# Kernel tuning notes

Hardware: AMD Instinct MI355X
Metric: run time of the kernel (lower is better)

The kernel has to match this reference:

```python
import jax, jax.numpy as jnp
import numpy as np

B, S, D, R, N, H = 2, 2048, 1024, 64, 16, 16
DH = D // H  # 64


def setup_inputs() -> dict:
    key = jax.random.key(0)
    ks = jax.random.split(key, 16)
    inp = {
        "x": jax.random.normal(ks[0], (B, S, D), dtype=jnp.float32),
        "feature_q_w": jax.random.uniform(ks[1], (B, S, N), dtype=jnp.float32),
        "feature_k_w": jax.random.uniform(ks[2], (B, S, N), dtype=jnp.float32),
        "feature_v_w": jax.random.uniform(ks[3], (B, S, N), dtype=jnp.float32),
        "restore_q_w": jax.random.uniform(ks[4], (B, S, N), dtype=jnp.float32),
        "restore_k_w": jax.random.uniform(ks[5], (B, S, N), dtype=jnp.float32),
        "restore_v_w": jax.random.uniform(ks[6], (B, S, N), dtype=jnp.float32),
        # expert parameter pools (per-expert low-rank projections)
        "f_q": jax.random.normal(ks[7], (N, D, R), dtype=jnp.float32) / np.sqrt(D),
        "f_k": jax.random.normal(ks[8], (N, D, R), dtype=jnp.float32) / np.sqrt(D),
        "f_v": jax.random.normal(ks[9], (N, D, R), dtype=jnp.float32) / np.sqrt(D),
        "r_q": jax.random.normal(ks[10], (N, R, D), dtype=jnp.float32) / np.sqrt(R),
        "r_k": jax.random.normal(ks[11], (N, R, D), dtype=jnp.float32) / np.sqrt(R),
        "r_v": jax.random.normal(ks[12], (N, R, D), dtype=jnp.float32) / np.sqrt(R),
        # expand_O: nn.Linear(D, D, bias=False) weight, shape [D_out, D_in]
        "W_O": jax.random.normal(ks[13], (D, D), dtype=jnp.float32) / np.sqrt(D),
    }
    return inp


def _compress(w, F_pool, x):
    # math-equivalent to einsum('bsn,ndr->bsdr') then ('bsd,bsdr->bsr')
    # reordered to avoid the [B,S,D,R] intermediate: [B,S,N,R] instead.
    t = jnp.einsum('bsd,ndr->bsnr', x, F_pool)
    return jnp.einsum('bsn,bsnr->bsr', w, t)


def _restore(w, R_pool, h):
    # math-equivalent to einsum('bsn,nrd->bsrd') then ('bsr,bsrd->bsd')
    mix = jnp.einsum('bsr,bsn->bsnr', h, w)  # small [B,S,N,R]
    return jnp.einsum('bsnr,nrd->bsd', mix, R_pool)


def reference(x, feature_q_w, feature_k_w, feature_v_w,
              restore_q_w, restore_k_w, restore_v_w,
              f_q, f_k, f_v, r_q, r_k, r_v, W_O):
    b, s, d = x.shape
    h_q = _compress(feature_q_w, f_q, x)
    h_k = _compress(feature_k_w, f_k, x)
    h_v = _compress(feature_v_w, f_v, x)
    Q = _restore(restore_q_w, r_q, h_q)
    K = _restore(restore_k_w, r_k, h_k)
    V = _restore(restore_v_w, r_v, h_v)
    # split heads: [B,H,S,DH]
    Q = Q.reshape(b, s, H, DH).transpose(0, 2, 1, 3)
    K = K.reshape(b, s, H, DH).transpose(0, 2, 1, 3)
    V = V.reshape(b, s, H, DH).transpose(0, 2, 1, 3)
    scale = 1.0 / np.sqrt(DH)
    scores = jnp.einsum('bhqd,bhkd->bhqk', Q, K) * scale
    causal = jnp.tril(jnp.ones((s, s), dtype=bool))
    scores = jnp.where(causal, scores, jnp.float32(-1e9))
    attn = jax.nn.softmax(scores, axis=-1)
    out = jnp.einsum('bhqk,bhkd->bhqd', attn, V)
    out = out.transpose(0, 2, 1, 3).reshape(b, s, d)
    # nn.Linear(bias=False): y = x @ W_O.T
    return out @ W_O.T
```

## Files before the change

### kernel.cpp

```cpp
#include <hip/hip_runtime.h>

#define BS   4096
#define DD   1024
#define SEQ  2048
#define SLAB (BS * DD)
#define POOL (16 * 64 * 1024)

typedef unsigned short u16;
typedef __attribute__((ext_vector_type(8))) short  s16x8;
typedef __attribute__((ext_vector_type(4))) float  f32x4;

__device__ __forceinline__ u16 f2bf(float x) {
    unsigned u = __float_as_uint(x);
    return (u16)((u + 0x7fffu + ((u >> 16) & 1u)) >> 16);
}
__device__ __forceinline__ float bf2f(u16 h) { return __uint_as_float(((unsigned)h) << 16); }
__device__ __forceinline__ void bsplit(float x, u16& h, u16& l) {
    h = f2bf(x);
    l = f2bf(x - bf2f(h));
}

__global__ __launch_bounds__(256) void convert_ew(
    const float* __restrict__ in, u16* __restrict__ oh, u16* __restrict__ ol, int n4)
{
    for (int i = blockIdx.x * 256 + threadIdx.x; i < n4; i += gridDim.x * 256) {
        float4 v = ((const float4*)in)[i];
        u16 h0,h1,h2,h3, l0,l1,l2,l3;
        bsplit(v.x,h0,l0); bsplit(v.y,h1,l1); bsplit(v.z,h2,l2); bsplit(v.w,h3,l3);
        u16* ph = oh + i * 4; ph[0]=h0; ph[1]=h1; ph[2]=h2; ph[3]=h3;
        u16* pl = ol + i * 4; pl[0]=l0; pl[1]=l1; pl[2]=l2; pl[3]=l3;
    }
}

__global__ __launch_bounds__(256) void convert_tr3(
    const float* __restrict__ in0, const float* __restrict__ in1, const float* __restrict__ in2,
    u16* __restrict__ oh, u16* __restrict__ ol, int Rows, int Cols, int zPerPool)
{
    __shared__ float ts[64][65];
    const int z = blockIdx.z, pool = z / zPerPool, zi = z % zPerPool;
    const float* in = (pool == 0 ? in0 : (pool == 1 ? in1 : in2)) + (size_t)zi * Rows * Cols;
    const size_t obase = (size_t)z * Rows * Cols;
    const int r0 = blockIdx.x * 64, c0 = blockIdx.y * 64;
    const int t = threadIdx.x;

    const int rr = t >> 4, c4 = (t & 15) * 4;
    #pragma unroll
    for (int i = 0; i < 4; ++i) {
        int r = i * 16 + rr;
        float4 v = *(const float4*)&in[(size_t)(r0 + r) * Cols + c0 + c4];
        ts[r][c4+0] = v.x; ts[r][c4+1] = v.y; ts[r][c4+2] = v.z; ts[r][c4+3] = v.w;
    }
    __syncthreads();
    const int cc = t >> 4, rq = (t & 15) * 4;
    #pragma unroll
    for (int i = 0; i < 4; ++i) {
        int c = i * 16 + cc;
        size_t o = obase + (size_t)(c0 + c) * Rows + r0 + rq;
        #pragma unroll
        for (int j = 0; j < 4; ++j) {
            u16 h, l; bsplit(ts[rq + j][c], h, l);
            oh[o + j] = h; ol[o + j] = l;
        }
    }
}

template<int OMODE>
__global__ __launch_bounds__(256, 3) void gemm_split(
    const u16* __restrict__ Ah, const u16* __restrict__ Al,
    const u16* __restrict__ Bh, const u16* __restrict__ Bl,
    float* __restrict__ Cf, u16* __restrict__ Ch, u16* __restrict__ Cl,
    long aZ, long bZ, long cZ, int K, int lda, int ldb, int ldc)
{
    __shared__ u16 sBh[128][32], sBl[128][32];

    const int t = threadIdx.x, wave = t >> 6, lane = t & 63;
    const int m0 = blockIdx.x * 128, n0 = blockIdx.y * 128;
    const long z = blockIdx.z;
    Ah += z * aZ; Al += z * aZ; Bh += z * bZ; Bl += z * bZ;

    const int lr = lane >> 2, lk = (lane & 3) * 8;
    const u16* gBh = Bh + (size_t)(n0 + wave * 16 + lr) * ldb + lk;
    const u16* gBl = Bl + (size_t)(n0 + wave * 16 + lr) * ldb + lk;

    const int fr = lane & 15, fk = (lane >> 4) * 8;
    const u16* gAh = Ah + (size_t)(m0 + (wave >> 1) * 64 + fr) * lda + fk;
    const u16* gAl = Al + (size_t)(m0 + (wave >> 1) * 64 + fr) * lda + fk;

    f32x4 acc[4][4];
    #pragma unroll
    for (int i = 0; i < 4; ++i)
        #pragma unroll
        for (int j = 0; j < 4; ++j) acc[i][j] = (f32x4){0.f, 0.f, 0.f, 0.f};

    const int br = (wave & 1) * 64 + fr;

    for (int k0 = 0; k0 < K; k0 += 32) {
        #define STG(g, s, ld) do { \
            __builtin_amdgcn_global_load_lds( \
                (const __attribute__((address_space(1))) void*)(g + k0), \
                (__attribute__((address_space(3))) void*)&s[wave * 16][0], 16, 0, 0); \
            __builtin_amdgcn_global_load_lds( \
                (const __attribute__((address_space(1))) void*)(g + k0 + (size_t)64 * ld), \
                (__attribute__((address_space(3))) void*)&s[wave * 16 + 64][0], 16, 0, 0); \
        } while (0)
        STG(gBh, sBh, ldb); STG(gBl, sBl, ldb);
        #undef STG

        s16x8 ahf[4], alf[4];
        #pragma unroll
        for (int i = 0; i < 4; ++i) {
            ahf[i] = *(const s16x8*)&gAh[(size_t)(16 * i) * lda + k0];
            alf[i] = *(const s16x8*)&gAl[(size_t)(16 * i) * lda + k0];
        }
        __syncthreads();

        #pragma unroll
        for (int j = 0; j < 4; ++j) {
            s16x8 bh = *(const s16x8*)&sBh[br + 16 * j][fk];
            s16x8 bl = *(const s16x8*)&sBl[br + 16 * j][fk];
            #pragma unroll
            for (int i = 0; i < 4; ++i)
                acc[i][j] = __builtin_amdgcn_mfma_f32_16x16x32_bf16(ahf[i], bh, acc[i][j], 0, 0, 0);
            #pragma unroll
            for (int i = 0; i < 4; ++i)
                acc[i][j] = __builtin_amdgcn_mfma_f32_16x16x32_bf16(ahf[i], bl, acc[i][j], 0, 0, 0);
            #pragma unroll
            for (int i = 0; i < 4; ++i)
                acc[i][j] = __builtin_amdgcn_mfma_f32_16x16x32_bf16(alf[i], bh, acc[i][j], 0, 0, 0);
        }
        __syncthreads();
    }

    const int row0 = m0 + (wave >> 1) * 64 + (lane >> 4) * 4;
    const int col0 = n0 + (wave & 1) * 64 + fr;
    if constexpr (OMODE == 0) {
        Cf += z * cZ;
        #pragma unroll
        for (int i = 0; i < 4; ++i)
            #pragma unroll
            for (int j = 0; j < 4; ++j)
                #pragma unroll
                for (int r = 0; r < 4; ++r)
                    Cf[(size_t)(row0 + 16 * i + r) * ldc + col0 + 16 * j] = acc[i][j][r];
    } else {
        Ch += z * cZ; Cl += z * cZ;
        #pragma unroll
        for (int i = 0; i < 4; ++i)
            #pragma unroll
            for (int j = 0; j < 4; ++j)
                #pragma unroll
                for (int r = 0; r < 4; ++r) {
                    u16 h, l; bsplit(acc[i][j][r], h, l);
                    size_t o = (size_t)(row0 + 16 * i + r) * ldc + col0 + 16 * j;
                    Ch[o] = h; Cl[o] = l;
                }
    }
}

__global__ __launch_bounds__(256) void mix3(
    u16* __restrict__ Th, u16* __restrict__ Tl,
    const float* fw0, const float* fw1, const float* fw2,
    const float* rw0, const float* rw1, const float* rw2)
{
    const int p = blockIdx.y;
    const float* fw = p == 0 ? fw0 : (p == 1 ? fw1 : fw2);
    const float* rw = p == 0 ? rw0 : (p == 1 ? rw1 : rw2);
    u16* th = Th + (size_t)p * SLAB;
    u16* tl = Tl + (size_t)p * SLAB;

    const int t = threadIdx.x;
    const int bs = blockIdx.x * 4 + (t >> 6);
    const int r = t & 63;
    const float* fwp = fw + bs * 16;
    const float* rwp = rw + bs * 16;
    u16* rowh = th + (size_t)bs * DD + r;
    u16* rowl = tl + (size_t)bs * DD + r;

    float h = 0.f;
    #pragma unroll
    for (int n = 0; n < 16; ++n) h += fwp[n] * (bf2f(rowh[n * 64]) + bf2f(rowl[n * 64]));
    #pragma unroll
    for (int n = 0; n < 16; ++n) {
        u16 hh, ll; bsplit(rwp[n] * h, hh, ll);
        rowh[n * 64] = hh; rowl[n * 64] = ll;
    }
}

__global__ __launch_bounds__(256) void attn_mfma(
    const u16* __restrict__ Qh, const u16* __restrict__ Ql,
    const u16* __restrict__ Kh, const u16* __restrict__ Kl,
    const u16* __restrict__ Vh, const u16* __restrict__ Vl,
    u16* __restrict__ Oh, u16* __restrict__ Ol)
{
    __shared__ u16 sKh[64][64], sKl[64][64];
    __shared__ u16 sVh[64][64], sVl[64][64];
    __shared__ u16 sPh[128][64], sPl[128][64];

    const int t = threadIdx.x, w = t >> 6, lane = t & 63;
    const int g = blockIdx.x;
    const int u = g & 255, v = g >> 8;
    const int bh = (v << 4) + (u >> 4);
    const int bx = v ? (15 - (u & 15)) : (u & 15);
    const int b = bh >> 4, h = bh & 15;
    const int q0 = bx * 128;
    const int l15 = lane & 15, l4 = lane >> 4;

    s16x8 qfh[2][2], qfl[2][2];
    #pragma unroll
    for (int fi = 0; fi < 2; ++fi) {
        int qr = q0 + w * 32 + fi * 16 + l15;
        size_t base = ((size_t)(b * SEQ + qr)) * DD + h * 64;
        #pragma unroll
        for (int dk = 0; dk < 2; ++dk) {
            qfh[fi][dk] = *(const s16x8*)&Qh[base + dk * 32 + l4 * 8];
            qfl[fi][dk] = *(const s16x8*)&Ql[base + dk * 32 + l4 * 8];
        }
    }

    f32x4 oacc[2][4];
    #pragma unroll
    for (int fi = 0; fi < 2; ++fi)
        #pragma unroll
        for (int dj = 0; dj < 4; ++dj) oacc[fi][dj] = (f32x4){0.f,0.f,0.f,0.f};
    float mrow[2][4], lrow[2][4];
    #pragma unroll
    for (int fi = 0; fi < 2; ++fi)
        #pragma unroll
        for (int r = 0; r < 4; ++r) { mrow[fi][r] = -1e30f; lrow[fi][r] = 0.f; }

    const int ntiles = 2 * bx + 2;
    for (int kt = 0; kt < ntiles; ++kt) {
        __syncthreads();
        #pragma unroll
        for (int it = 0; it < 2; ++it) {
            int id = it * 256 + t;
            int kr = id >> 3, dg = (id & 7) * 8;
            size_t gaddr = ((size_t)(b * SEQ + kt * 64 + kr)) * DD + h * 64 + dg;
            s16x8 kh8 = *(const s16x8*)&Kh[gaddr];
            s16x8 kl8 = *(const s16x8*)&Kl[gaddr];
            int kbyte = (dg * 2) ^ ((kr & 7) << 4);
            *(s16x8*)((char*)&sKh[kr][0] + kbyte) = kh8;
            *(s16x8*)((char*)&sKl[kr][0] + kbyte) = kl8;
            s16x8 vh8 = *(const s16x8*)&Vh[gaddr];
            s16x8 vl8 = *(const s16x8*)&Vl[gaddr];
            #pragma unroll
            for (int j = 0; j < 8; ++j) {
                int d = dg + j;
                int vbyte = (kr * 2) ^ ((d & 7) << 4);
                *(u16*)((char*)&sVh[d][0] + vbyte) = (u16)vh8[j];
                *(u16*)((char*)&sVl[d][0] + vbyte) = (u16)vl8[j];
            }
        }
        __syncthreads();

        f32x4 s[2][4];
        #pragma unroll
        for (int fi = 0; fi < 2; ++fi)
            #pragma unroll
            for (int fj = 0; fj < 4; ++fj) s[fi][fj] = (f32x4){0.f,0.f,0.f,0.f};
        #pragma unroll
        for (int fj = 0; fj < 4; ++fj) {
            int krow = fj * 16 + l15;
            #pragma unroll
            for (int dk = 0; dk < 2; ++dk) {
                int byte = ((dk * 32 + l4 * 8) * 2) ^ ((krow & 7) << 4);
                s16x8 kbh = *(const s16x8*)((const char*)&sKh[krow][0] + byte);
                s16x8 kbl = *(const s16x8*)((const char*)&sKl[krow][0] + byte);
                #pragma unroll
                for (int fi = 0; fi < 2; ++fi) {
                    s[fi][fj] = __builtin_amdgcn_mfma_f32_16x16x32_bf16(qfh[fi][dk], kbh, s[fi][fj], 0,0,0);
                    s[fi][fj] = __builtin_amdgcn_mfma_f32_16x16x32_bf16(qfh[fi][dk], kbl, s[fi][fj], 0,0,0);
                    s[fi][fj] = __builtin_amdgcn_mfma_f32_16x16x32_bf16(qfl[fi][dk], kbh, s[fi][fj], 0,0,0);
                }
            }
        }

        #pragma unroll
        for (int fi = 0; fi < 2; ++fi) {
            int qrow = q0 + w * 32 + fi * 16 + l4 * 4;
            #pragma unroll
            for (int fj = 0; fj < 4; ++fj) {
                int kcol = kt * 64 + fj * 16 + l15;
                #pragma unroll
                for (int r = 0; r < 4; ++r)
                    s[fi][fj][r] = (kcol > qrow + r) ? -1e9f : s[fi][fj][r] * 0.125f;
            }
        }

        #pragma unroll
        for (int fi = 0; fi < 2; ++fi) {
            f32x4 pm = s[fi][0];
            #pragma unroll
            for (int fj = 1; fj < 4; ++fj)
                #pragma unroll
                for (int r = 0; r < 4; ++r) pm[r] = fmaxf(pm[r], s[fi][fj][r]);
            #pragma unroll
            for (int st = 1; st < 16; st <<= 1)
                #pragma unroll
                for (int r = 0; r < 4; ++r) pm[r] = fmaxf(pm[r], __shfl_xor(pm[r], st));

            float al[4];
            #pragma unroll
            for (int r = 0; r < 4; ++r) {
                float mn = fmaxf(mrow[fi][r], pm[r]);
                al[r] = __expf(mrow[fi][r] - mn);
                mrow[fi][r] = mn;
            }
            f32x4 rs = (f32x4){0.f,0.f,0.f,0.f};
            #pragma unroll
            for (int fj = 0; fj < 4; ++fj) {
                #pragma unroll
                for (int r = 0; r < 4; ++r) {
                    float p = __expf(s[fi][fj][r] - mrow[fi][r]);
                    rs[r] += p;
                    u16 ph, pl; bsplit(p, ph, pl);
                    int prow = w * 32 + fi * 16 + l4 * 4 + r;
                    int byte = ((fj * 16 + l15) * 2) ^ ((prow & 7) << 4);
                    *(u16*)((char*)&sPh[prow][0] + byte) = ph;
                    *(u16*)((char*)&sPl[prow][0] + byte) = pl;
                }
            }
            #pragma unroll
            for (int st = 1; st < 16; st <<= 1)
                #pragma unroll
                for (int r = 0; r < 4; ++r) rs[r] += __shfl_xor(rs[r], st);
            #pragma unroll
            for (int r = 0; r < 4; ++r) {
                lrow[fi][r] = lrow[fi][r] * al[r] + rs[r];
                #pragma unroll
                for (int dj = 0; dj < 4; ++dj) oacc[fi][dj][r] *= al[r];
            }
        }

        #pragma unroll
        for (int kk = 0; kk < 2; ++kk) {
            s16x8 pah[2], pal[2];
            #pragma unroll
            for (int fi = 0; fi < 2; ++fi) {
                int prow = w * 32 + fi * 16 + l15;
                int byte = ((kk * 32 + l4 * 8) * 2) ^ ((prow & 7) << 4);
                pah[fi] = *(const s16x8*)((const char*)&sPh[prow][0] + byte);
                pal[fi] = *(const s16x8*)((const char*)&sPl[prow][0] + byte);
            }
            #pragma unroll
            for (int dj = 0; dj < 4; ++dj) {
                int vrow = dj * 16 + l15;
                int byte = ((kk * 32 + l4 * 8) * 2) ^ ((vrow & 7) << 4);
                s16x8 vbh = *(const s16x8*)((const char*)&sVh[vrow][0] + byte);
                s16x8 vbl = *(const s16x8*)((const char*)&sVl[vrow][0] + byte);
                #pragma unroll
                for (int fi = 0; fi < 2; ++fi) {
                    oacc[fi][dj] = __builtin_amdgcn_mfma_f32_16x16x32_bf16(pah[fi], vbh, oacc[fi][dj], 0,0,0);
                    oacc[fi][dj] = __builtin_amdgcn_mfma_f32_16x16x32_bf16(pah[fi], vbl, oacc[fi][dj], 0,0,0);
                    oacc[fi][dj] = __builtin_amdgcn_mfma_f32_16x16x32_bf16(pal[fi], vbh, oacc[fi][dj], 0,0,0);
                }
            }
        }
    }

    #pragma unroll
    for (int fi = 0; fi < 2; ++fi)
        #pragma unroll
        for (int r = 0; r < 4; ++r) {
            int qr = q0 + w * 32 + fi * 16 + l4 * 4 + r;
            size_t base = ((size_t)(b * SEQ + qr)) * DD + h * 64;
            float inv = 1.0f / lrow[fi][r];
            #pragma unroll
            for (int dj = 0; dj < 4; ++dj) {
                u16 hh, ll; bsplit(oacc[fi][dj][r] * inv, hh, ll);
                Oh[base + dj * 16 + l15] = hh;
                Ol[base + dj * 16 + l15] = ll;
            }
        }
}

extern "C" void kernel_launch(void* const* d_in, const int* in_sizes, int n_in,
                              void* d_out, int out_size, void* d_ws, size_t ws_size,
                              hipStream_t stream)
{
    const float* x     = (const float*)d_in[0];
    const float* fw[3] = { (const float*)d_in[1], (const float*)d_in[2], (const float*)d_in[3] };
    const float* rw[3] = { (const float*)d_in[4], (const float*)d_in[5], (const float*)d_in[6] };
    const float* fp[3] = { (const float*)d_in[7], (const float*)d_in[8], (const float*)d_in[9] };
    const float* rp[3] = { (const float*)d_in[10], (const float*)d_in[11], (const float*)d_in[12] };
    const float* Wo    = (const float*)d_in[13];
    float* out = (float*)d_out;

    u16* U    = (u16*)d_ws;
    u16* xh   = U;                  u16* xl   = xh  + SLAB;
    u16* fTh  = xl   + SLAB;        u16* fTl  = fTh + 3 * POOL;
    u16* rTh  = fTl  + 3 * POOL;    u16* rTl  = rTh + 3 * POOL;
    u16* Wh   = rTl  + 3 * POOL;    u16* Wl   = Wh  + POOL;
    u16* Th   = Wl   + POOL;        u16* Tl   = Th  + 3 * SLAB;
    u16* QKVh = Tl   + 3 * SLAB;    u16* QKVl = QKVh + 3 * SLAB;
    u16* Ohb  = xh;                 u16* Olb  = xl;

    dim3 blk(256);

    convert_ew<<<dim3(4096), blk, 0, stream>>>(x,  xh, xl, SLAB / 4);
    convert_ew<<<dim3(1024), blk, 0, stream>>>(Wo, Wh, Wl, (DD * DD) / 4);
    convert_tr3<<<dim3(16, 1, 48), blk, 0, stream>>>(fp[0], fp[1], fp[2], fTh, fTl, 1024, 64, 16);
    convert_tr3<<<dim3(16, 16, 3), blk, 0, stream>>>(rp[0], rp[1], rp[2], rTh, rTl, 1024, 1024, 1);

    gemm_split<1><<<dim3(32, 8, 3), blk, 0, stream>>>(
        xh, xl, fTh, fTl, nullptr, Th, Tl, 0, POOL, SLAB, DD, DD, DD, DD);

    mix3<<<dim3(BS / 4, 3), blk, 0, stream>>>(
        Th, Tl, fw[0], fw[1], fw[2], rw[0], rw[1], rw[2]);

    gemm_split<1><<<dim3(32, 8, 3), blk, 0, stream>>>(
        Th, Tl, rTh, rTl, nullptr, QKVh, QKVl, SLAB, POOL, SLAB, DD, DD, DD, DD);

    attn_mfma<<<dim3(512), blk, 0, stream>>>(
        QKVh, QKVl, QKVh + SLAB, QKVl + SLAB, QKVh + 2 * SLAB, QKVl + 2 * SLAB,
        Ohb, Olb);

    gemm_split<0><<<dim3(32, 8, 1), blk, 0, stream>>>(
        Ohb, Olb, Wh, Wl, out, nullptr, nullptr, 0, 0, 0, DD, DD, DD, DD);
}
```

Measured before the change: 637.4 us.

## Write V transposed from projection GEMM and read K/V directly from global in attention

```diff
diff --git a/kernel.cpp b/kernel.cpp
--- a/kernel.cpp
+++ b/kernel.cpp
@@ -69,7 +69,7 @@
     const u16* __restrict__ Ah, const u16* __restrict__ Al,
     const u16* __restrict__ Bh, const u16* __restrict__ Bl,
     float* __restrict__ Cf, u16* __restrict__ Ch, u16* __restrict__ Cl,
-    long aZ, long bZ, long cZ, int K, int lda, int ldb, int ldc)
+    long aZ, long bZ, long cZ, int K, int lda, int ldb, int ldc, int vtrans)
 {
     __shared__ u16 sBh[128][32], sBl[128][32];
 
@@ -144,16 +144,37 @@
                     Cf[(size_t)(row0 + 16 * i + r) * ldc + col0 + 16 * j] = acc[i][j][r];
     } else {
         Ch += z * cZ; Cl += z * cZ;
-        #pragma unroll
-        for (int i = 0; i < 4; ++i)
-            #pragma unroll
-            for (int j = 0; j < 4; ++j)
-                #pragma unroll
-                for (int r = 0; r < 4; ++r) {
-                    u16 h, l; bsplit(acc[i][j][r], h, l);
-                    size_t o = (size_t)(row0 + 16 * i + r) * ldc + col0 + 16 * j;
-                    Ch[o] = h; Cl[o] = l;
+        if (vtrans && z == 2) {
+            const int b_ = m0 >> 11;
+            const int h_ = (n0 + (wave & 1) * 64) >> 6;
+            #pragma unroll
+            for (int i = 0; i < 4; ++i) {
+                int srow = (m0 & (SEQ - 1)) + (wave >> 1) * 64 + (lane >> 4) * 4 + 16 * i;
+                #pragma unroll
+                for (int j = 0; j < 4; ++j) {
+                    int d = fr + 16 * j;
+                    size_t o = ((size_t)((b_ * 16 + h_) * 64 + d)) * SEQ + srow;
+                    ushort4 hv, lv;
+                    bsplit(acc[i][j][0], hv.x, lv.x);
+                    bsplit(acc[i][j][1], hv.y, lv.y);
+                    bsplit(acc[i][j][2], hv.z, lv.z);
+                    bsplit(acc[i][j][3], hv.w, lv.w);
+                    *(ushort4*)&Ch[o] = hv;
+                    *(ushort4*)&Cl[o] = lv;
                 }
+            }
+        } else {
+            #pragma unroll
+            for (int i = 0; i < 4; ++i)
+                #pragma unroll
+                for (int j = 0; j < 4; ++j)
+                    #pragma unroll
+                    for (int r = 0; r < 4; ++r) {
+                        u16 h, l; bsplit(acc[i][j][r], h, l);
+                        size_t o = (size_t)(row0 + 16 * i + r) * ldc + col0 + 16 * j;
+                        Ch[o] = h; Cl[o] = l;
+                    }
+        }
     }
 }
 
@@ -189,11 +210,9 @@
 __global__ __launch_bounds__(256) void attn_mfma(
     const u16* __restrict__ Qh, const u16* __restrict__ Ql,
     const u16* __restrict__ Kh, const u16* __restrict__ Kl,
-    const u16* __restrict__ Vh, const u16* __restrict__ Vl,
+    const u16* __restrict__ Vth, const u16* __restrict__ Vtl,
     u16* __restrict__ Oh, u16* __restrict__ Ol)
 {
-    __shared__ u16 sKh[64][64], sKl[64][64];
-    __shared__ u16 sVh[64][64], sVl[64][64];
     __shared__ u16 sPh[128][64], sPl[128][64];
 
     const int t = threadIdx.x, w = t >> 6, lane = t & 63;
@@ -230,29 +249,6 @@
 
     const int ntiles = 2 * bx + 2;
     for (int kt = 0; kt < ntiles; ++kt) {
-        __syncthreads();
-        #pragma unroll
-        for (int it = 0; it < 2; ++it) {
-            int id = it * 256 + t;
-            int kr = id >> 3, dg = (id & 7) * 8;
-            size_t gaddr = ((size_t)(b * SEQ + kt * 64 + kr)) * DD + h * 64 + dg;
-            s16x8 kh8 = *(const s16x8*)&Kh[gaddr];
-            s16x8 kl8 = *(const s16x8*)&Kl[gaddr];
-            int kbyte = (dg * 2) ^ ((kr & 7) << 4);
-            *(s16x8*)((char*)&sKh[kr][0] + kbyte) = kh8;
-            *(s16x8*)((char*)&sKl[kr][0] + kbyte) = kl8;
-            s16x8 vh8 = *(const s16x8*)&Vh[gaddr];
-            s16x8 vl8 = *(const s16x8*)&Vl[gaddr];
-            #pragma unroll
-            for (int j = 0; j < 8; ++j) {
-                int d = dg + j;
-                int vbyte = (kr * 2) ^ ((d & 7) << 4);
-                *(u16*)((char*)&sVh[d][0] + vbyte) = (u16)vh8[j];
-                *(u16*)((char*)&sVl[d][0] + vbyte) = (u16)vl8[j];
-            }
-        }
-        __syncthreads();
-
         f32x4 s[2][4];
         #pragma unroll
         for (int fi = 0; fi < 2; ++fi)
@@ -260,12 +256,11 @@
             for (int fj = 0; fj < 4; ++fj) s[fi][fj] = (f32x4){0.f,0.f,0.f,0.f};
         #pragma unroll
         for (int fj = 0; fj < 4; ++fj) {
-            int krow = fj * 16 + l15;
+            size_t kbase = ((size_t)(b * SEQ + kt * 64 + fj * 16 + l15)) * DD + h * 64;
             #pragma unroll
             for (int dk = 0; dk < 2; ++dk) {
-                int byte = ((dk * 32 + l4 * 8) * 2) ^ ((krow & 7) << 4);
-                s16x8 kbh = *(const s16x8*)((const char*)&sKh[krow][0] + byte);
-                s16x8 kbl = *(const s16x8*)((const char*)&sKl[krow][0] + byte);
+                s16x8 kbh = *(const s16x8*)&Kh[kbase + dk * 32 + l4 * 8];
+                s16x8 kbl = *(const s16x8*)&Kl[kbase + dk * 32 + l4 * 8];
                 #pragma unroll
                 for (int fi = 0; fi < 2; ++fi) {
                     s[fi][fj] = __builtin_amdgcn_mfma_f32_16x16x32_bf16(qfh[fi][dk], kbh, s[fi][fj], 0,0,0);
@@ -344,10 +339,9 @@
             }
             #pragma unroll
             for (int dj = 0; dj < 4; ++dj) {
-                int vrow = dj * 16 + l15;
-                int byte = ((kk * 32 + l4 * 8) * 2) ^ ((vrow & 7) << 4);
-                s16x8 vbh = *(const s16x8*)((const char*)&sVh[vrow][0] + byte);
-                s16x8 vbl = *(const s16x8*)((const char*)&sVl[vrow][0] + byte);
+                size_t vbase = ((size_t)(bh * 64 + dj * 16 + l15)) * SEQ + kt * 64 + kk * 32 + l4 * 8;
+                s16x8 vbh = *(const s16x8*)&Vth[vbase];
+                s16x8 vbl = *(const s16x8*)&Vtl[vbase];
                 #pragma unroll
                 for (int fi = 0; fi < 2; ++fi) {
                     oacc[fi][dj] = __builtin_amdgcn_mfma_f32_16x16x32_bf16(pah[fi], vbh, oacc[fi][dj], 0,0,0);
@@ -403,18 +397,18 @@
     convert_tr3<<<dim3(16, 16, 3), blk, 0, stream>>>(rp[0], rp[1], rp[2], rTh, rTl, 1024, 1024, 1);
 
     gemm_split<1><<<dim3(32, 8, 3), blk, 0, stream>>>(
-        xh, xl, fTh, fTl, nullptr, Th, Tl, 0, POOL, SLAB, DD, DD, DD, DD);
+        xh, xl, fTh, fTl, nullptr, Th, Tl, 0, POOL, SLAB, DD, DD, DD, DD, 0);
 
     mix3<<<dim3(BS / 4, 3), blk, 0, stream>>>(
         Th, Tl, fw[0], fw[1], fw[2], rw[0], rw[1], rw[2]);
 
     gemm_split<1><<<dim3(32, 8, 3), blk, 0, stream>>>(
-        Th, Tl, rTh, rTl, nullptr, QKVh, QKVl, SLAB, POOL, SLAB, DD, DD, DD, DD);
+        Th, Tl, rTh, rTl, nullptr, QKVh, QKVl, SLAB, POOL, SLAB, DD, DD, DD, DD, 1);
 
     attn_mfma<<<dim3(512), blk, 0, stream>>>(
         QKVh, QKVl, QKVh + SLAB, QKVl + SLAB, QKVh + 2 * SLAB, QKVl + 2 * SLAB,
         Ohb, Olb);
 
     gemm_split<0><<<dim3(32, 8, 1), blk, 0, stream>>>(
-        Ohb, Olb, Wh, Wl, out, nullptr, nullptr, 0, 0, 0, DD, DD, DD, DD);
-}
+        Ohb, Olb, Wh, Wl, out, nullptr, nullptr, 0, 0, 0, DD, DD, DD, DD, 0);
+}
```

After: 672.7 us. 1.06x slower.
